# Kernel optimization log

Hardware: AMD Instinct MI355X
Metric: run time of the kernel (lower is better)

## Reference

```python
import jax, jax.numpy as jnp
import numpy as np

B, L, D, H, E = 8, 256, 128, 6, 32

def setup_inputs() -> dict:
    key = jax.random.key(0)
    ks = jax.random.split(key, 9)
    s = 0.02
    return {
        "x": jax.random.normal(ks[0], (B, L, D), jnp.float32),
        "weight_adj": jax.random.uniform(ks[1], (B, H, L, L), jnp.float32),
        "e": jax.random.normal(ks[2], (B, L, L, E), jnp.float32),
        "W_w": jax.random.normal(ks[3], (D, D), jnp.float32) * s,
        "W_b": jax.random.normal(ks[4], (D,), jnp.float32) * s,
        "Wx_w": jax.random.normal(ks[5], (H, H + 2 * D + E), jnp.float32) * s,
        "Wx_b": jax.random.normal(ks[6], (H,), jnp.float32) * s,
        "Wxx_w": jax.random.normal(ks[7], (D, D), jnp.float32) * s,
        "Wxx_b": jax.random.normal(ks[8], (D,), jnp.float32) * s,
    }

def reference(x, weight_adj, e, W_w, W_b, Wx_w, Wx_b, Wxx_w, Wxx_b):
    d = x.shape[-1]
    h = weight_adj.shape[1]
    # mean over heads, then graph conv + linear + relu
    adj_avg = weight_adj.mean(axis=1)                      # [B,L,L]
    gcn = jax.nn.relu(jnp.einsum('bij,bjd->bid', adj_avg, x) @ W_w.T + W_b)  # [B,L,d]
    # Wx applied to cat([weight_adj_perm, node_i, node_j, e], -1), decomposed
    # column-wise so the huge [B,L,L,2d+H+E] concat is never materialized;
    # math is identical to Linear(cat(...)).
    Wa  = Wx_w[:, :h]                 # [H,H]
    Wn1 = Wx_w[:, h:h + d]            # [H,d]
    Wn2 = Wx_w[:, h + d:h + 2 * d]    # [H,d]
    We  = Wx_w[:, h + 2 * d:]         # [H,E]
    adj_term = jnp.einsum('bhij,kh->bijk', weight_adj, Wa)   # [B,L,L,H]
    n1 = gcn @ Wn1.T                                          # [B,L,H] (row node)
    n2 = gcn @ Wn2.T                                          # [B,L,H] (col node)
    e_term = jnp.einsum('bije,ke->bijk', e, We)               # [B,L,L,H]
    new_adj = adj_term + n1[:, :, None, :] + n2[:, None, :, :] + e_term + Wx_b
    new_adj = jnp.transpose(new_adj, (0, 3, 1, 2))            # [B,H,L,L]
    out = gcn @ Wxx_w.T + Wxx_b                               # [B,L,d]
    return out, new_adj
```

## Files before the change

kernel.cpp:

```cpp
#include <hip/hip_runtime.h>

#define Bn 8
#define Ln 256
#define Dn 128
#define Hn 6
#define En 32
#define WXROW (Hn + 2*Dn + En)
#define ROWS 4

__global__ __launch_bounds__(256) void k_gcn(
    const float* __restrict__ x, const float* __restrict__ wadj,
    const float* __restrict__ W_w, const float* __restrict__ W_b,
    const float* __restrict__ Wx_w,
    const float* __restrict__ Wxx_w, const float* __restrict__ Wxx_b,
    float* __restrict__ out, float* __restrict__ n1_ws, float* __restrict__ n2_ws)
{
    __shared__ float adj[ROWS][Ln];
    __shared__ float part[8][ROWS][Dn];
    __shared__ float t_s[ROWS][Dn];
    __shared__ float g_s[ROWS][Dn];

    const int t  = threadIdx.x;
    const int b  = blockIdx.x >> 6;
    const int i0 = (blockIdx.x & 63) * ROWS;

    {
        const int r  = t >> 6;
        const int j4 = t & 63;
        const float4* w4 = (const float4*)wadj;
        float4 sum = {0.f, 0.f, 0.f, 0.f};
        #pragma unroll
        for (int h = 0; h < Hn; ++h) {
            const float4 v = w4[(((size_t)b * Hn + h) * Ln + (i0 + r)) * (Ln / 4) + j4];
            sum.x += v.x; sum.y += v.y; sum.z += v.z; sum.w += v.w;
        }
        const float inv_h = 1.0f / 6.0f;
        sum.x *= inv_h; sum.y *= inv_h; sum.z *= inv_h; sum.w *= inv_h;
        ((float4*)&adj[0][0])[r * (Ln / 4) + j4] = sum;
    }
    __syncthreads();

    {
        const int q  = t >> 5;
        const int d4 = t & 31;
        float4 acc[ROWS];
        #pragma unroll
        for (int r = 0; r < ROWS; ++r) acc[r] = {0.f, 0.f, 0.f, 0.f};

        const float4* xp4 = (const float4*)(x + (size_t)b * Ln * Dn) + d4;
        const float4* adj4 = (const float4*)&adj[0][0];
        const int j0 = q * 32;

        #pragma unroll 2
        for (int jj4 = 0; jj4 < 8; ++jj4) {
            const int j = j0 + jj4 * 4;
            const float4 xv0 = xp4[(size_t)(j + 0) * 32];
            const float4 xv1 = xp4[(size_t)(j + 1) * 32];
            const float4 xv2 = xp4[(size_t)(j + 2) * 32];
            const float4 xv3 = xp4[(size_t)(j + 3) * 32];
            #pragma unroll
            for (int r = 0; r < ROWS; ++r) {
                const float4 a = adj4[r * (Ln / 4) + (j >> 2)];
                float4 v = acc[r];
                v.x = fmaf(a.x, xv0.x, v.x); v.y = fmaf(a.x, xv0.y, v.y);
                v.z = fmaf(a.x, xv0.z, v.z); v.w = fmaf(a.x, xv0.w, v.w);
                v.x = fmaf(a.y, xv1.x, v.x); v.y = fmaf(a.y, xv1.y, v.y);
                v.z = fmaf(a.y, xv1.z, v.z); v.w = fmaf(a.y, xv1.w, v.w);
                v.x = fmaf(a.z, xv2.x, v.x); v.y = fmaf(a.z, xv2.y, v.y);
                v.z = fmaf(a.z, xv2.z, v.z); v.w = fmaf(a.z, xv2.w, v.w);
                v.x = fmaf(a.w, xv3.x, v.x); v.y = fmaf(a.w, xv3.y, v.y);
                v.z = fmaf(a.w, xv3.z, v.z); v.w = fmaf(a.w, xv3.w, v.w);
                acc[r] = v;
            }
        }
        #pragma unroll
        for (int r = 0; r < ROWS; ++r)
            ((float4*)&part[q][r][0])[d4] = acc[r];
    }
    __syncthreads();

    {
        const int d  = t & 127;
        const int rr = t >> 7;
        #pragma unroll
        for (int rq = 0; rq < 2; ++rq) {
            const int r = rr + rq * 2;
            float s = 0.f;
            #pragma unroll
            for (int q = 0; q < 8; ++q) s += part[q][r][d];
            t_s[r][d] = s;
        }
    }
    __syncthreads();

    {
        const int s = t >> 7, d = t & 127;
        const int r0 = s, r1 = s + 2;
        float a0 = W_b[d], a1 = a0;
        const float4* wr = (const float4*)(W_w + (size_t)d * Dn);
        const float4* t0 = (const float4*)&t_s[r0][0];
        const float4* t1 = (const float4*)&t_s[r1][0];
        #pragma unroll 8
        for (int c4 = 0; c4 < Dn / 4; ++c4) {
            const float4 w = wr[c4];
            const float4 u0 = t0[c4];
            const float4 u1 = t1[c4];
            a0 = fmaf(u0.x, w.x, a0); a0 = fmaf(u0.y, w.y, a0);
            a0 = fmaf(u0.z, w.z, a0); a0 = fmaf(u0.w, w.w, a0);
            a1 = fmaf(u1.x, w.x, a1); a1 = fmaf(u1.y, w.y, a1);
            a1 = fmaf(u1.z, w.z, a1); a1 = fmaf(u1.w, w.w, a1);
        }
        g_s[r0][d] = fmaxf(a0, 0.f);
        g_s[r1][d] = fmaxf(a1, 0.f);
    }
    __syncthreads();

    {
        const int s = t >> 7, d = t & 127;
        const int r0 = s, r1 = s + 2;
        float a0 = Wxx_b[d], a1 = a0;
        const float4* wr = (const float4*)(Wxx_w + (size_t)d * Dn);
        const float4* g0 = (const float4*)&g_s[r0][0];
        const float4* g1 = (const float4*)&g_s[r1][0];
        #pragma unroll 8
        for (int c4 = 0; c4 < Dn / 4; ++c4) {
            const float4 w = wr[c4];
            const float4 u0 = g0[c4];
            const float4 u1 = g1[c4];
            a0 = fmaf(u0.x, w.x, a0); a0 = fmaf(u0.y, w.y, a0);
            a0 = fmaf(u0.z, w.z, a0); a0 = fmaf(u0.w, w.w, a0);
            a1 = fmaf(u1.x, w.x, a1); a1 = fmaf(u1.y, w.y, a1);
            a1 = fmaf(u1.z, w.z, a1); a1 = fmaf(u1.w, w.w, a1);
        }
        out[((size_t)b * Ln + (i0 + r0)) * Dn + d] = a0;
        out[((size_t)b * Ln + (i0 + r1)) * Dn + d] = a1;
    }

    if (t < ROWS * 2 * Hn) {
        const int r  = t / (2 * Hn);
        const int kk = t % (2 * Hn);
        const int k  = (kk < Hn) ? kk : (kk - Hn);
        const bool isn2 = (kk >= Hn);
        const float* wrow = Wx_w + (size_t)k * WXROW + Hn + (isn2 ? Dn : 0);
        float acc = 0.f;
        #pragma unroll 8
        for (int c = 0; c < Dn; ++c)
            acc = fmaf(g_s[r][c], wrow[c], acc);
        const size_t idx = ((size_t)b * Hn + k) * Ln + (i0 + r);
        if (isn2) n2_ws[idx] = acc;
        else      n1_ws[idx] = acc;
    }
}

#define EPAD 33
__global__ __launch_bounds__(256) void k_adj(
    const float* __restrict__ wadj, const float* __restrict__ e,
    const float* __restrict__ Wx_w, const float* __restrict__ Wx_b,
    const float* __restrict__ n1_ws, const float* __restrict__ n2_ws,
    float* __restrict__ new_adj)
{
    __shared__ float e_lds[Ln * EPAD];
    __shared__ float Wa_s[Hn][Hn];
    __shared__ float We_s[Hn][En];
    __shared__ float bias_n1[Hn];

    const int t = threadIdx.x;
    const int b = blockIdx.x >> 8;
    const int i = blockIdx.x & 255;

    if (t < Hn * Hn) {
        const int k = t / Hn, h = t % Hn;
        Wa_s[k][h] = Wx_w[(size_t)k * WXROW + h];
    }
    if (t >= 64 && t < 64 + Hn * En) {
        const int q = t - 64, k = q / En, c = q % En;
        We_s[k][c] = Wx_w[(size_t)k * WXROW + Hn + 2 * Dn + c];
    }
    if (t >= 32 && t < 32 + Hn) {
        const int k = t - 32;
        bias_n1[k] = Wx_b[k] + n1_ws[((size_t)b * Hn + k) * Ln + i];
    }

    {
        const float4* ep4 = (const float4*)(e + (((size_t)b * Ln + i) * Ln) * En);
        #pragma unroll
        for (int k = 0; k < 8; ++k) {
            const int idx = t + k * 256;
            const float4 v = ep4[idx];
            const int j = idx >> 3;
            const int c = (idx & 7) * 4;
            float* dst = &e_lds[j * EPAD + c];
            dst[0] = v.x; dst[1] = v.y; dst[2] = v.z; dst[3] = v.w;
        }
    }
    __syncthreads();

    const int j = t;

    float ev[En];
    {
        const float* src = &e_lds[j * EPAD];
        #pragma unroll
        for (int c = 0; c < En; ++c) ev[c] = src[c];
    }

    float wv[Hn];
    #pragma unroll
    for (int h = 0; h < Hn; ++h)
        wv[h] = wadj[(((size_t)b * Hn + h) * Ln + i) * Ln + j];

    float n2v[Hn];
    #pragma unroll
    for (int k = 0; k < Hn; ++k)
        n2v[k] = n2_ws[((size_t)b * Hn + k) * Ln + j];

    #pragma unroll
    for (int k = 0; k < Hn; ++k) {
        float acc = bias_n1[k] + n2v[k];
        #pragma unroll
        for (int h = 0; h < Hn; ++h)
            acc = fmaf(wv[h], Wa_s[k][h], acc);
        #pragma unroll
        for (int c = 0; c < En; ++c)
            acc = fmaf(ev[c], We_s[k][c], acc);
        new_adj[(((size_t)b * Hn + k) * Ln + i) * Ln + j] = acc;
    }
}

extern "C" void kernel_launch(void* const* d_in, const int* in_sizes, int n_in,
                              void* d_out, int out_size, void* d_ws, size_t ws_size,
                              hipStream_t stream) {
    const float* x      = (const float*)d_in[0];
    const float* wadj   = (const float*)d_in[1];
    const float* e      = (const float*)d_in[2];
    const float* W_w    = (const float*)d_in[3];
    const float* W_b    = (const float*)d_in[4];
    const float* Wx_w   = (const float*)d_in[5];
    const float* Wx_b   = (const float*)d_in[6];
    const float* Wxx_w  = (const float*)d_in[7];
    const float* Wxx_b  = (const float*)d_in[8];

    float* out      = (float*)d_out;
    float* new_adj  = out + (size_t)Bn * Ln * Dn;

    float* n1_ws = (float*)d_ws;
    float* n2_ws = n1_ws + (size_t)Bn * Hn * Ln;

    k_gcn<<<Bn * (Ln / ROWS), 256, 0, stream>>>(x, wadj, W_w, W_b, Wx_w,
                                                Wxx_w, Wxx_b, out, n1_ws, n2_ws);
    k_adj<<<Bn * Ln, 256, 0, stream>>>(wadj, e, Wx_w, Wx_b, n1_ws, n2_ws, new_adj);
}
```

Baseline: 148.2 us.

## Drop LDS staging in k_adj and read e directly per thread

Removes the shared-memory staging of the e tile, the weight copies into LDS and the block barrier from k_adj. Each thread now reads its own 32-float e row with float4 loads and reads the weights through uniform (scalar) global loads, and launch bounds request 8 waves per SIMD. The aim is to free the roughly 33KB of LDS per block, raise occupancy, and remove the sync and LDS round trip. The cost is that per-thread e loads stride 128 bytes across lanes, so they are less coalesced than the old cooperative load.

```diff
diff --git a/kernel.cpp b/kernel.cpp
--- a/kernel.cpp
+++ b/kernel.cpp
@@ -152,79 +152,49 @@
     }
 }
 
-#define EPAD 33
-__global__ __launch_bounds__(256) void k_adj(
+__global__ __launch_bounds__(256, 8) void k_adj(
     const float* __restrict__ wadj, const float* __restrict__ e,
     const float* __restrict__ Wx_w, const float* __restrict__ Wx_b,
     const float* __restrict__ n1_ws, const float* __restrict__ n2_ws,
     float* __restrict__ new_adj)
 {
-    __shared__ float e_lds[Ln * EPAD];
-    __shared__ float Wa_s[Hn][Hn];
-    __shared__ float We_s[Hn][En];
-    __shared__ float bias_n1[Hn];
-
     const int t = threadIdx.x;
     const int b = blockIdx.x >> 8;
     const int i = blockIdx.x & 255;
-
-    if (t < Hn * Hn) {
-        const int k = t / Hn, h = t % Hn;
-        Wa_s[k][h] = Wx_w[(size_t)k * WXROW + h];
-    }
-    if (t >= 64 && t < 64 + Hn * En) {
-        const int q = t - 64, k = q / En, c = q % En;
-        We_s[k][c] = Wx_w[(size_t)k * WXROW + Hn + 2 * Dn + c];
-    }
-    if (t >= 32 && t < 32 + Hn) {
-        const int k = t - 32;
-        bias_n1[k] = Wx_b[k] + n1_ws[((size_t)b * Hn + k) * Ln + i];
-    }
-
-    {
-        const float4* ep4 = (const float4*)(e + (((size_t)b * Ln + i) * Ln) * En);
-        #pragma unroll
-        for (int k = 0; k < 8; ++k) {
-            const int idx = t + k * 256;
-            const float4 v = ep4[idx];
-            const int j = idx >> 3;
-            const int c = (idx & 7) * 4;
-            float* dst = &e_lds[j * EPAD + c];
-            dst[0] = v.x; dst[1] = v.y; dst[2] = v.z; dst[3] = v.w;
-        }
-    }
-    __syncthreads();
-
     const int j = t;
 
-    float ev[En];
-    {
-        const float* src = &e_lds[j * EPAD];
-        #pragma unroll
-        for (int c = 0; c < En; ++c) ev[c] = src[c];
-    }
-
-    float wv[Hn];
-    #pragma unroll
-    for (int h = 0; h < Hn; ++h)
-        wv[h] = wadj[(((size_t)b * Hn + h) * Ln + i) * Ln + j];
-
-    float n2v[Hn];
+    float acc[Hn];
+    #pragma unroll
+    for (int k = 0; k < Hn; ++k) {
+        const float bias = Wx_b[k] + n1_ws[((size_t)b * Hn + k) * Ln + i];
+        acc[k] = bias + n2_ws[((size_t)b * Hn + k) * Ln + j];
+    }
+
+    #pragma unroll
+    for (int h = 0; h < Hn; ++h) {
+        const float wv = wadj[(((size_t)b * Hn + h) * Ln + i) * Ln + j];
+        #pragma unroll
+        for (int k = 0; k < Hn; ++k)
+            acc[k] = fmaf(wv, Wx_w[(size_t)k * WXROW + h], acc[k]);
+    }
+
+    const float4* ep4 = (const float4*)(e + (((size_t)b * Ln + i) * Ln + j) * En);
+    #pragma unroll
+    for (int c4 = 0; c4 < En / 4; ++c4) {
+        const float4 ev = ep4[c4];
+        #pragma unroll
+        for (int k = 0; k < Hn; ++k) {
+            const float* wr = Wx_w + (size_t)k * WXROW + Hn + 2 * Dn + c4 * 4;
+            acc[k] = fmaf(ev.x, wr[0], acc[k]);
+            acc[k] = fmaf(ev.y, wr[1], acc[k]);
+            acc[k] = fmaf(ev.z, wr[2], acc[k]);
+            acc[k] = fmaf(ev.w, wr[3], acc[k]);
+        }
+    }
+
     #pragma unroll
     for (int k = 0; k < Hn; ++k)
-        n2v[k] = n2_ws[((size_t)b * Hn + k) * Ln + j];
-
-    #pragma unroll
-    for (int k = 0; k < Hn; ++k) {
-        float acc = bias_n1[k] + n2v[k];
-        #pragma unroll
-        for (int h = 0; h < Hn; ++h)
-            acc = fmaf(wv[h], Wa_s[k][h], acc);
-        #pragma unroll
-        for (int c = 0; c < En; ++c)
-            acc = fmaf(ev[c], We_s[k][c], acc);
-        new_adj[(((size_t)b * Hn + k) * Ln + i) * Ln + j] = acc;
-    }
+        new_adj[(((size_t)b * Hn + k) * Ln + i) * Ln + j] = acc[k];
 }
 
 extern "C" void kernel_launch(void* const* d_in, const int* in_sizes, int n_in,
```

Measured after the change: 153.5 us. 1.04x slower.

## Split k_adj across column halves and output heads, drop LDS weight staging

Applied to the files above, without the earlier changes.

Each k_adj block now covers half of the j columns (128) for one (b,i) row. Its two thread halves each compute three of the six output heads, which doubles the grid and halves the e tile held in LDS. The Wa/We/bias LDS staging and its setup are removed, so weights are read directly from global memory as uniform loads. A launch_bounds occupancy hint of 8 blocks per CU is added. The aim is more parallelism and occupancy for this memory-bound kernel, at the cost of each wadj/e element being loaded by two threads and extra scalar weight reads.

```diff
diff --git a/kernel.cpp b/kernel.cpp
--- a/kernel.cpp
+++ b/kernel.cpp
@@ -153,53 +153,42 @@
 }
 
 #define EPAD 33
-__global__ __launch_bounds__(256) void k_adj(
+__global__ __launch_bounds__(256, 8) void k_adj(
     const float* __restrict__ wadj, const float* __restrict__ e,
     const float* __restrict__ Wx_w, const float* __restrict__ Wx_b,
     const float* __restrict__ n1_ws, const float* __restrict__ n2_ws,
     float* __restrict__ new_adj)
 {
-    __shared__ float e_lds[Ln * EPAD];
-    __shared__ float Wa_s[Hn][Hn];
-    __shared__ float We_s[Hn][En];
-    __shared__ float bias_n1[Hn];
-
-    const int t = threadIdx.x;
-    const int b = blockIdx.x >> 8;
-    const int i = blockIdx.x & 255;
-
-    if (t < Hn * Hn) {
-        const int k = t / Hn, h = t % Hn;
-        Wa_s[k][h] = Wx_w[(size_t)k * WXROW + h];
-    }
-    if (t >= 64 && t < 64 + Hn * En) {
-        const int q = t - 64, k = q / En, c = q % En;
-        We_s[k][c] = Wx_w[(size_t)k * WXROW + Hn + 2 * Dn + c];
-    }
-    if (t >= 32 && t < 32 + Hn) {
-        const int k = t - 32;
-        bias_n1[k] = Wx_b[k] + n1_ws[((size_t)b * Hn + k) * Ln + i];
-    }
-
-    {
-        const float4* ep4 = (const float4*)(e + (((size_t)b * Ln + i) * Ln) * En);
-        #pragma unroll
-        for (int k = 0; k < 8; ++k) {
+    __shared__ float e_lds[128 * EPAD];
+
+    const int t  = threadIdx.x;
+    const int bi = blockIdx.x >> 1;
+    const int jh = blockIdx.x & 1;
+    const int b  = bi >> 8;
+    const int i  = bi & 255;
+    const int j0 = jh << 7;
+
+    {
+        const float4* ep4 = (const float4*)(e + (((size_t)b * Ln + i) * Ln + j0) * En);
+        #pragma unroll
+        for (int k = 0; k < 4; ++k) {
             const int idx = t + k * 256;
             const float4 v = ep4[idx];
-            const int j = idx >> 3;
-            const int c = (idx & 7) * 4;
-            float* dst = &e_lds[j * EPAD + c];
+            const int jl = idx >> 3;
+            const int c  = (idx & 7) * 4;
+            float* dst = &e_lds[jl * EPAD + c];
             dst[0] = v.x; dst[1] = v.y; dst[2] = v.z; dst[3] = v.w;
         }
     }
     __syncthreads();
 
-    const int j = t;
+    const int jl = t & 127;
+    const int kh = t >> 7;
+    const int j  = j0 + jl;
 
     float ev[En];
     {
-        const float* src = &e_lds[j * EPAD];
+        const float* src = &e_lds[jl * EPAD];
         #pragma unroll
         for (int c = 0; c < En; ++c) ev[c] = src[c];
     }
@@ -209,20 +198,18 @@
     for (int h = 0; h < Hn; ++h)
         wv[h] = wadj[(((size_t)b * Hn + h) * Ln + i) * Ln + j];
 
-    float n2v[Hn];
     #pragma unroll
-    for (int k = 0; k < Hn; ++k)
-        n2v[k] = n2_ws[((size_t)b * Hn + k) * Ln + j];
-
-    #pragma unroll
-    for (int k = 0; k < Hn; ++k) {
-        float acc = bias_n1[k] + n2v[k];
+    for (int q = 0; q < 3; ++q) {
+        const int k = kh + 2 * q;
+        float acc = Wx_b[k] + n1_ws[((size_t)b * Hn + k) * Ln + i]
+                            + n2_ws[((size_t)b * Hn + k) * Ln + j];
         #pragma unroll
         for (int h = 0; h < Hn; ++h)
-            acc = fmaf(wv[h], Wa_s[k][h], acc);
+            acc = fmaf(wv[h], Wx_w[(size_t)k * WXROW + h], acc);
+        const float* wr = Wx_w + (size_t)k * WXROW + Hn + 2 * Dn;
         #pragma unroll
         for (int c = 0; c < En; ++c)
-            acc = fmaf(ev[c], We_s[k][c], acc);
+            acc = fmaf(ev[c], wr[c], acc);
         new_adj[(((size_t)b * Hn + k) * Ln + i) * Ln + j] = acc;
     }
 }
@@ -248,5 +235,5 @@
 
     k_gcn<<<Bn * (Ln / ROWS), 256, 0, stream>>>(x, wadj, W_w, W_b, Wx_w,
                                                 Wxx_w, Wxx_b, out, n1_ws, n2_ws);
-    k_adj<<<Bn * Ln, 256, 0, stream>>>(wadj, e, Wx_w, Wx_b, n1_ws, n2_ws, new_adj);
+    k_adj<<<Bn * Ln * 2, 256, 0, stream>>>(wadj, e, Wx_w, Wx_b, n1_ws, n2_ws, new_adj);
 }
```

Result: slower. 174.7 us (+17.9%).
